# Optimization experiments

Hardware: AMD Instinct MI355X
Metric: run time of the kernel (lower is better)

Reference implementation:

```python
import jax, jax.numpy as jnp
import numpy as np

NEG_SLOPE = 0.01  # torch nn.LeakyReLU default


def setup_inputs() -> dict:
    key = jax.random.key(0)
    k1, k2, k3, k4, k5 = jax.random.split(key, 5)
    B, C, N, O = 32, 512, 1024, 512
    x = jax.random.normal(k1, (B, C, N), dtype=jnp.float32)
    wq = jax.random.normal(k2, (C,), dtype=jnp.float32) * (1.0 / np.sqrt(C))
    wk = jax.random.normal(k3, (C,), dtype=jnp.float32) * (1.0 / np.sqrt(C))
    wm = jax.random.normal(k4, (O, C), dtype=jnp.float32) * (1.0 / np.sqrt(C))
    bm = jax.random.normal(k5, (O,), dtype=jnp.float32) * 0.01
    return {"x": x, "wq": wq, "wk": wk, "wm": wm, "bm": bm}


def reference(x, wq, wk, wm, bm):
    # x: [B, C, N]
    q = jnp.einsum('c,bcn->bn', wq, x)            # [B, N] (Conv1d C->1, k=1, no bias)
    k = jnp.einsum('c,bcn->bn', wk, x)            # [B, N]
    scores = q[:, None, :] + k[:, :, None]        # [B, N, N] additive broadcast
    scores = jnp.where(scores > 0, scores, NEG_SLOPE * scores)  # LeakyReLU
    att = jax.nn.softmax(scores, axis=-1)         # softmax over last dim
    agg = jnp.einsum('bcn,bmn->bcm', x, att)      # weighted aggregation [B, C, N]
    out = jnp.einsum('oc,bcm->bom', wm, agg) + bm[None, :, None]  # Conv1d k=1
    return jax.nn.relu(out)
```

## Files before the change

kernel.cpp:

```cpp
#include <hip/hip_runtime.h>
#include <hip/hip_fp16.h>


constexpr int B = 32, C = 512, N = 1024, O = 512;
constexpr float L2E = 1.4426950408889634f;

typedef _Float16 half8 __attribute__((ext_vector_type(8)));
typedef _Float16 half4v __attribute__((ext_vector_type(4)));
typedef float f32x4 __attribute__((ext_vector_type(4)));

#if __has_builtin(__builtin_amdgcn_exp2f)
#define EXP2(x) __builtin_amdgcn_exp2f(x)
#else
#define EXP2(x) exp2f(x)
#endif

__device__ __forceinline__ half8 cvt8(float4 a, float4 b) {
  half8 h;
  h[0] = (_Float16)a.x; h[1] = (_Float16)a.y; h[2] = (_Float16)a.z; h[3] = (_Float16)a.w;
  h[4] = (_Float16)b.x; h[5] = (_Float16)b.y; h[6] = (_Float16)b.z; h[7] = (_Float16)b.w;
  return h;
}

__global__ __launch_bounds__(256) void qk_kernel(const float* __restrict__ x,
    const float* __restrict__ wq, const float* __restrict__ wk,
    float* __restrict__ q, float* __restrict__ k) {
  int b = blockIdx.y;
  int l = threadIdx.x & 63;
  int cq = threadIdx.x >> 6;
  int n = blockIdx.x * 64 + l;
  const float* xp  = x + ((size_t)b * C + cq * 128) * N + n;
  const float* wqp = wq + cq * 128;
  const float* wkp = wk + cq * 128;
  float aq = 0.f, ak = 0.f;
#pragma unroll 8
  for (int c = 0; c < 128; ++c) {
    float v = xp[(size_t)c * N];
    aq += wqp[c] * v;
    ak += wkp[c] * v;
  }
  __shared__ float rq[4][64], rk[4][64];
  rq[cq][l] = aq;
  rk[cq][l] = ak;
  __syncthreads();
  if (threadIdx.x < 64) {
    float sq = (rq[0][l] + rq[1][l]) + (rq[2][l] + rq[3][l]);
    float sk = (rk[0][l] + rk[1][l]) + (rk[2][l] + rk[3][l]);
    q[b * N + blockIdx.x * 64 + l] = L2E * sq;
    k[b * N + blockIdx.x * 64 + l] = L2E * sk;
  }
}

__global__ __launch_bounds__(256) void qmax_kernel(const float* __restrict__ q,
                                                   float* __restrict__ qmax) {
  int b = blockIdx.x;
  int tid = threadIdx.x;
  float m = -1e30f;
  for (int n = tid; n < N; n += 256) m = fmaxf(m, q[b * N + n]);
#pragma unroll
  for (int off = 32; off > 0; off >>= 1) m = fmaxf(m, __shfl_down(m, off, 64));
  __shared__ float red[4];
  if ((tid & 63) == 0) red[tid >> 6] = m;
  __syncthreads();
  if (tid == 0) qmax[b] = fmaxf(fmaxf(red[0], red[1]), fmaxf(red[2], red[3]));
}

__global__ __launch_bounds__(256) void gemm_a_kernel(const float* __restrict__ x,
    const float* __restrict__ q, const float* __restrict__ k,
    const float* __restrict__ qmax, _Float16* __restrict__ aggT) {
  __shared__ __align__(16) _Float16 As[128 * 40];
  __shared__ __align__(16) _Float16 Es[128 * 40];
  __shared__ __align__(16) float qs[N];
  __shared__ float izs[128];
  int b = blockIdx.z;
  int m0 = blockIdx.x * 128;
  int c0 = blockIdx.y * 128;
  int t = threadIdx.x;
  int w = t >> 6, l = t & 63;
  int cw = w >> 1, mw = w & 1;
  int lm = l & 15, q8 = (l >> 4) * 8;

  *(float4*)&qs[t * 4] = *(const float4*)&q[b * N + t * 4];

  int m_l = t >> 1, nh = t & 1;
  float km = k[b * N + m0 + m_l];
  float qmv = qmax[b];
  float s0 = qmv + km;
  float M  = fmaxf(s0, 0.01f * s0);
  float k2 = km - M;
  float k3 = 0.01f * km - M;
  float Zp = 0.f;
  const float* xrow = x + ((size_t)b * C + c0 + m_l) * N + nh * 16;

  __syncthreads();

  f32x4 acc[4][4] = {};
  for (int n0 = 0; n0 < N; n0 += 32) {
    float4 x0 = *(const float4*)(xrow + n0);
    float4 x1 = *(const float4*)(xrow + n0 + 4);
    float4 x2 = *(const float4*)(xrow + n0 + 8);
    float4 x3 = *(const float4*)(xrow + n0 + 12);
    float e[16];
#pragma unroll
    for (int jj = 0; jj < 16; ++jj) {
      float qv = qs[n0 + nh * 16 + jj];
      float arg = fmaxf(qv + k2, fmaf(0.01f, qv, k3));
      e[jj] = EXP2(arg);
      Zp += e[jj];
    }
    half8 h0, h1;
#pragma unroll
    for (int jj = 0; jj < 8; ++jj) { h0[jj] = (_Float16)e[jj]; h1[jj] = (_Float16)e[jj + 8]; }

    __syncthreads();
    *(half8*)&As[m_l * 40 + nh * 16]     = cvt8(x0, x1);
    *(half8*)&As[m_l * 40 + nh * 16 + 8] = cvt8(x2, x3);
    *(half8*)&Es[m_l * 40 + nh * 16]     = h0;
    *(half8*)&Es[m_l * 40 + nh * 16 + 8] = h1;
    __syncthreads();

    half8 af[4], bf[4];
#pragma unroll
    for (int i = 0; i < 4; ++i)
      af[i] = *(const half8*)&As[(cw * 64 + i * 16 + lm) * 40 + q8];
#pragma unroll
    for (int j = 0; j < 4; ++j)
      bf[j] = *(const half8*)&Es[(mw * 64 + j * 16 + lm) * 40 + q8];
#pragma unroll
    for (int i = 0; i < 4; ++i)
#pragma unroll
      for (int j = 0; j < 4; ++j)
        acc[i][j] = __builtin_amdgcn_mfma_f32_16x16x32_f16(af[i], bf[j], acc[i][j], 0, 0, 0);
  }

  float Z = Zp + __shfl_xor(Zp, 1, 64);
  izs[m_l] = 1.0f / Z;
  __syncthreads();

  float izv[4];
#pragma unroll
  for (int j = 0; j < 4; ++j) izv[j] = izs[mw * 64 + j * 16 + lm];
#pragma unroll
  for (int i = 0; i < 4; ++i) {
    int c_b = c0 + cw * 64 + i * 16 + (l >> 4) * 4;
#pragma unroll
    for (int j = 0; j < 4; ++j) {
      int m_c = m0 + mw * 64 + j * 16 + lm;
      float iz = izv[j];
      half4v h;
      h[0] = (_Float16)(acc[i][j][0] * iz);
      h[1] = (_Float16)(acc[i][j][1] * iz);
      h[2] = (_Float16)(acc[i][j][2] * iz);
      h[3] = (_Float16)(acc[i][j][3] * iz);
      *(half4v*)&aggT[((size_t)b * N + m_c) * C + c_b] = h;
    }
  }
}

__global__ __launch_bounds__(256) void gemm_b_kernel(const _Float16* __restrict__ aggT,
    const float* __restrict__ wm, const float* __restrict__ bm,
    float* __restrict__ out) {
  __shared__ __align__(16) _Float16 Am[128 * 40];
  __shared__ __align__(16) _Float16 Wo[128 * 40];
  int b = blockIdx.z;
  int m0 = blockIdx.x * 128;
  int o0 = blockIdx.y * 128;
  int t = threadIdx.x;
  int w = t >> 6, l = t & 63;
  int mw = w >> 1, ow = w & 1;
  int lm = l & 15, q8 = (l >> 4) * 8;
  int row = t >> 2, off8 = (t & 3) * 8;

  f32x4 acc[4][4] = {};
  for (int c0 = 0; c0 < C; c0 += 32) {
    half8 a0 = *(const half8*)&aggT[((size_t)b * N + m0 + row) * C + c0 + off8];
    half8 a1 = *(const half8*)&aggT[((size_t)b * N + m0 + row + 64) * C + c0 + off8];
    float4 w0 = *(const float4*)&wm[(size_t)(o0 + row) * C + c0 + off8];
    float4 w1 = *(const float4*)&wm[(size_t)(o0 + row) * C + c0 + off8 + 4];
    float4 w2 = *(const float4*)&wm[(size_t)(o0 + row + 64) * C + c0 + off8];
    float4 w3 = *(const float4*)&wm[(size_t)(o0 + row + 64) * C + c0 + off8 + 4];
    __syncthreads();
    *(half8*)&Am[row * 40 + off8]        = a0;
    *(half8*)&Am[(row + 64) * 40 + off8] = a1;
    *(half8*)&Wo[row * 40 + off8]        = cvt8(w0, w1);
    *(half8*)&Wo[(row + 64) * 40 + off8] = cvt8(w2, w3);
    __syncthreads();

    half8 af[4], bf[4];
#pragma unroll
    for (int i = 0; i < 4; ++i)
      af[i] = *(const half8*)&Am[(mw * 64 + i * 16 + lm) * 40 + q8];
#pragma unroll
    for (int j = 0; j < 4; ++j)
      bf[j] = *(const half8*)&Wo[(ow * 64 + j * 16 + lm) * 40 + q8];
#pragma unroll
    for (int i = 0; i < 4; ++i)
#pragma unroll
      for (int j = 0; j < 4; ++j)
        acc[i][j] = __builtin_amdgcn_mfma_f32_16x16x32_f16(af[i], bf[j], acc[i][j], 0, 0, 0);
  }

  float bias[4];
#pragma unroll
  for (int j = 0; j < 4; ++j) bias[j] = bm[o0 + ow * 64 + j * 16 + lm];
#pragma unroll
  for (int i = 0; i < 4; ++i) {
    int m_b = m0 + mw * 64 + i * 16 + (l >> 4) * 4;
#pragma unroll
    for (int j = 0; j < 4; ++j) {
      int o_c = o0 + ow * 64 + j * 16 + lm;
      float4 r;
      r.x = fmaxf(acc[i][j][0] + bias[j], 0.f);
      r.y = fmaxf(acc[i][j][1] + bias[j], 0.f);
      r.z = fmaxf(acc[i][j][2] + bias[j], 0.f);
      r.w = fmaxf(acc[i][j][3] + bias[j], 0.f);
      *(float4*)&out[((size_t)b * O + o_c) * N + m_b] = r;
    }
  }
}

extern "C" void kernel_launch(void* const* d_in, const int* in_sizes, int n_in,
                              void* d_out, int out_size, void* d_ws, size_t ws_size,
                              hipStream_t stream) {
  const float* x  = (const float*)d_in[0];
  const float* wq = (const float*)d_in[1];
  const float* wk = (const float*)d_in[2];
  const float* wm = (const float*)d_in[3];
  const float* bm = (const float*)d_in[4];
  float* out = (float*)d_out;

  float* q    = (float*)d_ws;
  float* k    = q + B * N;
  float* qmax = k + B * N;
  _Float16* aggT = (_Float16*)(qmax + 64);

  qk_kernel<<<dim3(N / 64, B), 256, 0, stream>>>(x, wq, wk, q, k);
  qmax_kernel<<<dim3(B), 256, 0, stream>>>(q, qmax);
  gemm_a_kernel<<<dim3(N / 128, C / 128, B), 256, 0, stream>>>(x, q, k, qmax, aggT);
  gemm_b_kernel<<<dim3(N / 128, O / 128, B), 256, 0, stream>>>(aggT, wm, bm, out);
}
```

Before: 244.6 us.

## Reassociate GEMMs: project x by wm first, then apply attention weights

Reorders the two matmuls so x is first projected by wm into Y (fp16, stored [B,O,N]), and the attention weights are then applied to Y with the softmax normalization, bias and ReLU fused into the epilogue. The attention exponentials are no longer recomputed for each of the four C tiles but for each O tile, and the second GEMM reads fp16 Y instead of converting fp32 x in its inner loop. The first GEMM now transposes x into pair-interleaved shared memory. FLOP count is unchanged because O equals C, and the reassociation changes fp16 rounding.

```diff
diff --git a/kernel.cpp b/kernel.cpp
--- a/kernel.cpp
+++ b/kernel.cpp
@@ -1,5 +1,4 @@
 #include <hip/hip_runtime.h>
-#include <hip/hip_fp16.h>
 
 
 constexpr int B = 32, C = 512, N = 1024, O = 512;
@@ -7,6 +6,7 @@
 
 typedef _Float16 half8 __attribute__((ext_vector_type(8)));
 typedef _Float16 half4v __attribute__((ext_vector_type(4)));
+typedef _Float16 half2v __attribute__((ext_vector_type(2)));
 typedef float f32x4 __attribute__((ext_vector_type(4)));
 
 #if __has_builtin(__builtin_amdgcn_exp2f)
@@ -65,19 +65,100 @@
   if (tid == 0) qmax[b] = fmaxf(fmaxf(red[0], red[1]), fmaxf(red[2], red[3]));
 }
 
-__global__ __launch_bounds__(256) void gemm_a_kernel(const float* __restrict__ x,
-    const float* __restrict__ q, const float* __restrict__ k,
-    const float* __restrict__ qmax, _Float16* __restrict__ aggT) {
-  __shared__ __align__(16) _Float16 As[128 * 40];
-  __shared__ __align__(16) _Float16 Es[128 * 40];
-  __shared__ __align__(16) float qs[N];
-  __shared__ float izs[128];
-  int b = blockIdx.z;
-  int m0 = blockIdx.x * 128;
-  int c0 = blockIdx.y * 128;
+__global__ __launch_bounds__(256) void gemm_y_kernel(const float* __restrict__ x,
+    const float* __restrict__ wm, _Float16* __restrict__ Yt) {
+  __shared__ half2v Xs[16 * 130];
+  __shared__ __align__(16) _Float16 Ws[128 * 40];
+  int b  = blockIdx.y;
+  int n0 = blockIdx.x * 128;
+  int o0 = blockIdx.z * 128;
   int t = threadIdx.x;
   int w = t >> 6, l = t & 63;
-  int cw = w >> 1, mw = w & 1;
+  int nw = w >> 1, ow = w & 1;
+  int lm = l & 15, q8 = (l >> 4) * 8, q4 = (l >> 4) * 4;
+
+  int cp = t >> 4, ng = t & 15;
+  int wrow = t >> 2, woff = (t & 3) * 8;
+
+  f32x4 acc[4][4] = {};
+  for (int c0 = 0; c0 < C; c0 += 32) {
+    const float* xr = x + ((size_t)b * C + c0 + 2 * cp) * N + n0 + ng * 8;
+    float4 a0 = *(const float4*)(xr);
+    float4 a1 = *(const float4*)(xr + 4);
+    float4 b0 = *(const float4*)(xr + N);
+    float4 b1 = *(const float4*)(xr + N + 4);
+    const float* wr = wm + (size_t)(o0 + wrow) * C + c0 + woff;
+    float4 w0 = *(const float4*)(wr);
+    float4 w1 = *(const float4*)(wr + 4);
+    float4 w2 = *(const float4*)(wr + (size_t)64 * C);
+    float4 w3 = *(const float4*)(wr + (size_t)64 * C + 4);
+    __syncthreads();
+    {
+      half2v* xp = &Xs[cp * 130 + ng * 8];
+      xp[0] = half2v{(_Float16)a0.x, (_Float16)b0.x};
+      xp[1] = half2v{(_Float16)a0.y, (_Float16)b0.y};
+      xp[2] = half2v{(_Float16)a0.z, (_Float16)b0.z};
+      xp[3] = half2v{(_Float16)a0.w, (_Float16)b0.w};
+      xp[4] = half2v{(_Float16)a1.x, (_Float16)b1.x};
+      xp[5] = half2v{(_Float16)a1.y, (_Float16)b1.y};
+      xp[6] = half2v{(_Float16)a1.z, (_Float16)b1.z};
+      xp[7] = half2v{(_Float16)a1.w, (_Float16)b1.w};
+      *(half8*)&Ws[wrow * 40 + woff]        = cvt8(w0, w1);
+      *(half8*)&Ws[(wrow + 64) * 40 + woff] = cvt8(w2, w3);
+    }
+    __syncthreads();
+
+    half8 af[4], bf[4];
+#pragma unroll
+    for (int i = 0; i < 4; ++i) {
+      int nrow = nw * 64 + i * 16 + lm;
+#pragma unroll
+      for (int jp = 0; jp < 4; ++jp) {
+        half2v p = Xs[(q4 + jp) * 130 + nrow];
+        af[i][2 * jp]     = p[0];
+        af[i][2 * jp + 1] = p[1];
+      }
+    }
+#pragma unroll
+    for (int j = 0; j < 4; ++j)
+      bf[j] = *(const half8*)&Ws[(ow * 64 + j * 16 + lm) * 40 + q8];
+#pragma unroll
+    for (int i = 0; i < 4; ++i)
+#pragma unroll
+      for (int j = 0; j < 4; ++j)
+        acc[i][j] = __builtin_amdgcn_mfma_f32_16x16x32_f16(af[i], bf[j], acc[i][j], 0, 0, 0);
+  }
+
+#pragma unroll
+  for (int i = 0; i < 4; ++i) {
+    int n_b = n0 + nw * 64 + i * 16 + (l >> 4) * 4;
+#pragma unroll
+    for (int j = 0; j < 4; ++j) {
+      int o_c = o0 + ow * 64 + j * 16 + lm;
+      half4v h;
+      h[0] = (_Float16)acc[i][j][0];
+      h[1] = (_Float16)acc[i][j][1];
+      h[2] = (_Float16)acc[i][j][2];
+      h[3] = (_Float16)acc[i][j][3];
+      *(half4v*)&Yt[((size_t)b * O + o_c) * N + n_b] = h;
+    }
+  }
+}
+
+__global__ __launch_bounds__(256) void gemm_out_kernel(const _Float16* __restrict__ Yt,
+    const float* __restrict__ q, const float* __restrict__ k,
+    const float* __restrict__ qmax, const float* __restrict__ bm,
+    float* __restrict__ out) {
+  __shared__ __align__(16) float qs[N];
+  __shared__ __align__(16) _Float16 Es[128 * 40];
+  __shared__ __align__(16) _Float16 Ys[128 * 40];
+  __shared__ float izs[128];
+  int b  = blockIdx.y;
+  int o0 = blockIdx.x * 128;
+  int m0 = blockIdx.z * 128;
+  int t = threadIdx.x;
+  int w = t >> 6, l = t & 63;
+  int mw = w >> 1, ow = w & 1;
   int lm = l & 15, q8 = (l >> 4) * 8;
 
   *(float4*)&qs[t * 4] = *(const float4*)&q[b * N + t * 4];
@@ -88,44 +169,50 @@
   float s0 = qmv + km;
   float M  = fmaxf(s0, 0.01f * s0);
   float k2 = km - M;
-  float k3 = 0.01f * km - M;
+  float k3 = fmaf(0.01f, km, -M);
   float Zp = 0.f;
-  const float* xrow = x + ((size_t)b * C + c0 + m_l) * N + nh * 16;
-
+  int yrow = t >> 2, yoff = (t & 3) * 8;
   __syncthreads();
 
   f32x4 acc[4][4] = {};
-  for (int n0 = 0; n0 < N; n0 += 32) {
-    float4 x0 = *(const float4*)(xrow + n0);
-    float4 x1 = *(const float4*)(xrow + n0 + 4);
-    float4 x2 = *(const float4*)(xrow + n0 + 8);
-    float4 x3 = *(const float4*)(xrow + n0 + 12);
-    float e[16];
-#pragma unroll
-    for (int jj = 0; jj < 16; ++jj) {
-      float qv = qs[n0 + nh * 16 + jj];
-      float arg = fmaxf(qv + k2, fmaf(0.01f, qv, k3));
-      e[jj] = EXP2(arg);
-      Zp += e[jj];
+  for (int n0k = 0; n0k < N; n0k += 32) {
+    half8 y0 = *(const half8*)&Yt[((size_t)b * O + o0 + yrow) * N + n0k + yoff];
+    half8 y1 = *(const half8*)&Yt[((size_t)b * O + o0 + yrow + 64) * N + n0k + yoff];
+    float4 qv0 = *(const float4*)&qs[n0k + nh * 16];
+    float4 qv1 = *(const float4*)&qs[n0k + nh * 16 + 4];
+    float4 qv2 = *(const float4*)&qs[n0k + nh * 16 + 8];
+    float4 qv3 = *(const float4*)&qs[n0k + nh * 16 + 12];
+    float ev[16];
+    {
+      const float* qq = (const float*)&qv0;
+      float tmp[16] = {qv0.x, qv0.y, qv0.z, qv0.w, qv1.x, qv1.y, qv1.z, qv1.w,
+                       qv2.x, qv2.y, qv2.z, qv2.w, qv3.x, qv3.y, qv3.z, qv3.w};
+      (void)qq;
+#pragma unroll
+      for (int jj = 0; jj < 16; ++jj) {
+        float arg = fmaxf(tmp[jj] + k2, fmaf(0.01f, tmp[jj], k3));
+        ev[jj] = EXP2(arg);
+        Zp += ev[jj];
+      }
     }
     half8 h0, h1;
 #pragma unroll
-    for (int jj = 0; jj < 8; ++jj) { h0[jj] = (_Float16)e[jj]; h1[jj] = (_Float16)e[jj + 8]; }
-
-    __syncthreads();
-    *(half8*)&As[m_l * 40 + nh * 16]     = cvt8(x0, x1);
-    *(half8*)&As[m_l * 40 + nh * 16 + 8] = cvt8(x2, x3);
+    for (int jj = 0; jj < 8; ++jj) { h0[jj] = (_Float16)ev[jj]; h1[jj] = (_Float16)ev[jj + 8]; }
+
+    __syncthreads();
     *(half8*)&Es[m_l * 40 + nh * 16]     = h0;
     *(half8*)&Es[m_l * 40 + nh * 16 + 8] = h1;
+    *(half8*)&Ys[yrow * 40 + yoff]        = y0;
+    *(half8*)&Ys[(yrow + 64) * 40 + yoff] = y1;
     __syncthreads();
 
     half8 af[4], bf[4];
 #pragma unroll
     for (int i = 0; i < 4; ++i)
-      af[i] = *(const half8*)&As[(cw * 64 + i * 16 + lm) * 40 + q8];
+      af[i] = *(const half8*)&Es[(mw * 64 + i * 16 + lm) * 40 + q8];
 #pragma unroll
     for (int j = 0; j < 4; ++j)
-      bf[j] = *(const half8*)&Es[(mw * 64 + j * 16 + lm) * 40 + q8];
+      bf[j] = *(const half8*)&Ys[(ow * 64 + j * 16 + lm) * 40 + q8];
 #pragma unroll
     for (int i = 0; i < 4; ++i)
 #pragma unroll
@@ -137,83 +224,19 @@
   izs[m_l] = 1.0f / Z;
   __syncthreads();
 
-  float izv[4];
-#pragma unroll
-  for (int j = 0; j < 4; ++j) izv[j] = izs[mw * 64 + j * 16 + lm];
-#pragma unroll
-  for (int i = 0; i < 4; ++i) {
-    int c_b = c0 + cw * 64 + i * 16 + (l >> 4) * 4;
-#pragma unroll
-    for (int j = 0; j < 4; ++j) {
-      int m_c = m0 + mw * 64 + j * 16 + lm;
-      float iz = izv[j];
-      half4v h;
-      h[0] = (_Float16)(acc[i][j][0] * iz);
-      h[1] = (_Float16)(acc[i][j][1] * iz);
-      h[2] = (_Float16)(acc[i][j][2] * iz);
-      h[3] = (_Float16)(acc[i][j][3] * iz);
-      *(half4v*)&aggT[((size_t)b * N + m_c) * C + c_b] = h;
-    }
-  }
-}
-
-__global__ __launch_bounds__(256) void gemm_b_kernel(const _Float16* __restrict__ aggT,
-    const float* __restrict__ wm, const float* __restrict__ bm,
-    float* __restrict__ out) {
-  __shared__ __align__(16) _Float16 Am[128 * 40];
-  __shared__ __align__(16) _Float16 Wo[128 * 40];
-  int b = blockIdx.z;
-  int m0 = blockIdx.x * 128;
-  int o0 = blockIdx.y * 128;
-  int t = threadIdx.x;
-  int w = t >> 6, l = t & 63;
-  int mw = w >> 1, ow = w & 1;
-  int lm = l & 15, q8 = (l >> 4) * 8;
-  int row = t >> 2, off8 = (t & 3) * 8;
-
-  f32x4 acc[4][4] = {};
-  for (int c0 = 0; c0 < C; c0 += 32) {
-    half8 a0 = *(const half8*)&aggT[((size_t)b * N + m0 + row) * C + c0 + off8];
-    half8 a1 = *(const half8*)&aggT[((size_t)b * N + m0 + row + 64) * C + c0 + off8];
-    float4 w0 = *(const float4*)&wm[(size_t)(o0 + row) * C + c0 + off8];
-    float4 w1 = *(const float4*)&wm[(size_t)(o0 + row) * C + c0 + off8 + 4];
-    float4 w2 = *(const float4*)&wm[(size_t)(o0 + row + 64) * C + c0 + off8];
-    float4 w3 = *(const float4*)&wm[(size_t)(o0 + row + 64) * C + c0 + off8 + 4];
-    __syncthreads();
-    *(half8*)&Am[row * 40 + off8]        = a0;
-    *(half8*)&Am[(row + 64) * 40 + off8] = a1;
-    *(half8*)&Wo[row * 40 + off8]        = cvt8(w0, w1);
-    *(half8*)&Wo[(row + 64) * 40 + off8] = cvt8(w2, w3);
-    __syncthreads();
-
-    half8 af[4], bf[4];
-#pragma unroll
-    for (int i = 0; i < 4; ++i)
-      af[i] = *(const half8*)&Am[(mw * 64 + i * 16 + lm) * 40 + q8];
-#pragma unroll
-    for (int j = 0; j < 4; ++j)
-      bf[j] = *(const half8*)&Wo[(ow * 64 + j * 16 + lm) * 40 + q8];
-#pragma unroll
-    for (int i = 0; i < 4; ++i)
-#pragma unroll
-      for (int j = 0; j < 4; ++j)
-        acc[i][j] = __builtin_amdgcn_mfma_f32_16x16x32_f16(af[i], bf[j], acc[i][j], 0, 0, 0);
-  }
-
-  float bias[4];
-#pragma unroll
-  for (int j = 0; j < 4; ++j) bias[j] = bm[o0 + ow * 64 + j * 16 + lm];
 #pragma unroll
   for (int i = 0; i < 4; ++i) {
     int m_b = m0 + mw * 64 + i * 16 + (l >> 4) * 4;
+    float4 iz4 = *(const float4*)&izs[mw * 64 + i * 16 + (l >> 4) * 4];
 #pragma unroll
     for (int j = 0; j < 4; ++j) {
       int o_c = o0 + ow * 64 + j * 16 + lm;
+      float bias = bm[o_c];
       float4 r;
-      r.x = fmaxf(acc[i][j][0] + bias[j], 0.f);
-      r.y = fmaxf(acc[i][j][1] + bias[j], 0.f);
-      r.z = fmaxf(acc[i][j][2] + bias[j], 0.f);
-      r.w = fmaxf(acc[i][j][3] + bias[j], 0.f);
+      r.x = fmaxf(fmaf(acc[i][j][0], iz4.x, bias), 0.f);
+      r.y = fmaxf(fmaf(acc[i][j][1], iz4.y, bias), 0.f);
+      r.z = fmaxf(fmaf(acc[i][j][2], iz4.z, bias), 0.f);
+      r.w = fmaxf(fmaf(acc[i][j][3], iz4.w, bias), 0.f);
       *(float4*)&out[((size_t)b * O + o_c) * N + m_b] = r;
     }
   }
@@ -232,10 +255,10 @@
   float* q    = (float*)d_ws;
   float* k    = q + B * N;
   float* qmax = k + B * N;
-  _Float16* aggT = (_Float16*)(qmax + 64);
+  _Float16* Yt = (_Float16*)(qmax + 64);
 
   qk_kernel<<<dim3(N / 64, B), 256, 0, stream>>>(x, wq, wk, q, k);
   qmax_kernel<<<dim3(B), 256, 0, stream>>>(q, qmax);
-  gemm_a_kernel<<<dim3(N / 128, C / 128, B), 256, 0, stream>>>(x, q, k, qmax, aggT);
-  gemm_b_kernel<<<dim3(N / 128, O / 128, B), 256, 0, stream>>>(aggT, wm, bm, out);
-}
+  gemm_y_kernel<<<dim3(N / 128, B, O / 128), 256, 0, stream>>>(x, wm, Yt);
+  gemm_out_kernel<<<dim3(O / 128, B, N / 128), 256, 0, stream>>>(Yt, q, k, qmax, bm, out);
+}
```

Result: faster. 228.9 us (-6.4%).
